# Optimization experiments

Hardware: AMD Instinct MI355X
Metric: run time of the kernel (lower is better)

The kernel has to match this reference:

```python
import jax, jax.numpy as jnp
import numpy as np

_ICO_FACES0 = [
    [0,11,5],[0,5,1],[0,1,7],[0,7,10],[0,10,11],
    [1,5,9],[5,11,4],[11,10,2],[10,7,6],[7,1,8],
    [3,9,4],[3,4,2],[3,2,6],[3,6,8],[3,8,9],
    [4,9,5],[2,4,11],[6,2,10],[8,6,7],[9,8,1]]


def ico_sphere_np(level=1):
    t = (1.0 + 5.0 ** 0.5) / 2.0
    verts = np.array([[-1,t,0],[1,t,0],[-1,-t,0],[1,-t,0],
                      [0,-1,t],[0,1,t],[0,-1,-t],[0,1,-t],
                      [t,0,-1],[t,0,1],[-t,0,-1],[-t,0,1]], dtype=np.float64)
    verts = verts / np.linalg.norm(verts, axis=1, keepdims=True)
    faces = [list(f) for f in _ICO_FACES0]
    for _ in range(level):
        vlist = [v for v in verts]
        cache = {}
        def mid(a, b):
            k = (min(a, b), max(a, b))
            if k not in cache:
                v = vlist[a] + vlist[b]
                vlist.append(v / np.linalg.norm(v))
                cache[k] = len(vlist) - 1
            return cache[k]
        nf = []
        for a, b, c in faces:
            ab, bc, ca = mid(a, b), mid(b, c), mid(c, a)
            nf += [[a, ab, ca], [b, bc, ab], [c, ca, bc], [ab, bc, ca]]
        faces = nf
        verts = np.stack(vlist)
    return verts.astype(np.float32), np.array(faces, dtype=np.int32)


def make_template():
    verts, faces = ico_sphere_np(1)          # (42,3), (80,3)
    v = verts[None]                          # (1,42,3)
    vmin = v.min(axis=1, keepdims=True)
    vmax = v.max(axis=1, keepdims=True)
    center = (vmin + vmax) / 2.0
    scale = (vmax - vmin).max() / 2.0        # normalize_to_box
    tv = 1.4 * (v - center) / scale          # cage_size = 1.4
    return jnp.asarray(np.transpose(tv, (0, 2, 1))), jnp.asarray(faces)  # (1,3,42),(80,3)


def optimize_cage(cage, shape, distance=0.4, iters=100, step=0.01):
    # cage (1,3,C), shape (B,3,N)
    B = shape.shape[0]
    cage = jnp.broadcast_to(cage, (B,) + cage.shape[1:])
    def body(_, c):
        d = jnp.sqrt(jnp.sum((c[:, :, :, None] - shape[:, :, None, :]) ** 2, axis=1))  # (B,C,N)
        min_d = jnp.min(d, axis=2)                                                     # (B,C)
        upd = (min_d > distance).astype(c.dtype)
        return c + step * (-c) * upd[:, None, :]
    return jax.lax.fori_loop(0, iters, body, cage)


def mean_value_coordinates_3D(query, vertices, faces):
    # query (B,P,3), vertices (B,C,3), faces (F,3) shared across batch
    B, P, _ = query.shape
    C = vertices.shape[1]
    r1 = jnp.array([1, 2, 0]); r2 = jnp.array([2, 0, 1])
    uj = vertices[:, None] - query[:, :, None]            # (B,P,C,3)
    dj = jnp.linalg.norm(uj, axis=-1, keepdims=True)      # (B,P,C,1)
    uj = uj / dj
    ui = uj[:, :, faces]                                  # (B,P,F,3,3)
    li = jnp.linalg.norm(ui[:, :, :, r1] - ui[:, :, :, r2], axis=-1)  # (B,P,F,3)
    eps = 2e-5
    li = jnp.where(li >= 2, li - jax.lax.stop_gradient(li - (2 - eps)), li)
    li = jnp.where(li <= -2, li - jax.lax.stop_gradient(li + (2 - eps)), li)
    theta = 2.0 * jnp.arcsin(li / 2.0)                    # (B,P,F,3)
    h = jnp.sum(theta, axis=-1, keepdims=True) / 2.0      # (B,P,F,1)
    ci = 2.0 * jnp.sin(h) * jnp.sin(h - theta) / (jnp.sin(theta[..., r1]) * jnp.sin(theta[..., r2])) - 1.0
    ci = jnp.clip(ci, -1 + 1e-5, 1 - 1e-5)
    si = jnp.sign(jnp.linalg.det(ui))[..., None] * jnp.sqrt(1.0 - ci ** 2)  # (B,P,F,3)
    di = dj[..., 0][:, :, faces]                          # (B,P,F,3)
    wi = (theta - ci[..., r1] * theta[..., r2] - ci[..., r2] * theta[..., r1]) / (di * jnp.sin(theta[..., r1]) * si[..., r2])
    inside = (jnp.pi - h[..., 0]) < 1e-4                  # (B,P,F)
    any_inside = jnp.any(inside, axis=-1, keepdims=True)[..., None]  # (B,P,1,1)
    wi = jnp.where(any_inside, 0.0, wi)
    wi = jnp.where(inside[..., None], jnp.sin(theta) * di[..., r2] * di[..., r1], wi)
    # scatter face corners -> vertices (B,P,F*3) -> (B,P,C)
    wj = jnp.zeros((B, P, C), wi.dtype).at[:, :, faces.reshape(-1)].add(wi.reshape(B, P, -1))
    close = dj[..., 0] < 1e-8                             # (B,P,C)
    wj = jnp.where(jnp.any(close, axis=-1, keepdims=True), 0.0, wj)
    wj = jnp.where(close, 1.0, wj)
    sumWj = jnp.sum(wj, axis=-1, keepdims=True)
    sumWj = jnp.where(sumWj == 0, 1.0, sumWj)
    return wj / sumWj, wi


def setup_inputs() -> dict:
    key = jax.random.key(0)
    ks = jax.random.split(key, 12)
    B, N, FEAT = 16, 8192, 256
    template_vertices, faces = make_template()
    def lin(k, fi, fo):
        k1, k2 = jax.random.split(k)
        return (jax.random.normal(k1, (fi, fo), jnp.float32) / np.sqrt(fi).astype(np.float32),
                jax.random.normal(k2, (fo,), jnp.float32) * 0.01)
    W1, b1 = lin(ks[0], 2 * FEAT, 512)
    W2, b2 = lin(ks[1], 512, 512)
    W3, b3 = lin(ks[2], 512, 256)
    W4, b4 = lin(ks[3], 256, 42 * 3)
    return {
        'source_shape': jax.random.normal(ks[4], (B, 3, N), jnp.float32),
        'target_shape': jax.random.normal(ks[5], (B, 3, N), jnp.float32),
        'source_f': jax.random.normal(ks[6], (B, FEAT), jnp.float32),
        'target_f': jax.random.normal(ks[7], (B, FEAT), jnp.float32),
        'template_vertices': template_vertices, 'faces': faces,
        'W1': W1, 'b1': b1, 'W2': W2, 'b2': b2, 'W3': W3, 'b3': b3, 'W4': W4, 'b4': b4,
    }


def reference(source_shape, target_shape, source_f, target_f, template_vertices, faces,
              W1, b1, W2, b2, W3, b3, W4, b4):
    B = source_shape.shape[0]
    cage = optimize_cage(template_vertices, source_shape)        # (B,3,42)
    feat = jnp.concatenate([source_f, target_f], axis=-1)        # (B,512)
    h = jax.nn.relu(feat @ W1 + b1)
    h = jax.nn.relu(h @ W2 + b2)
    h = jax.nn.relu(h @ W3 + b3)
    influence_offset = h @ W4 + b4                               # (B,126)
    cage_offset = influence_offset.reshape(B, 3, -1)             # (B,3,42)
    new_cage = cage + cage_offset
    cage_t = jnp.transpose(cage, (0, 2, 1))                      # (B,42,3)
    new_cage_t = jnp.transpose(new_cage, (0, 2, 1))
    weights, _ = mean_value_coordinates_3D(jnp.transpose(source_shape, (0, 2, 1)), cage_t, faces)
    weights = jax.lax.stop_gradient(weights)                     # weights.detach() in deform_with_MVC
    deformed = jnp.einsum('bpc,bcd->bpd', weights, new_cage_t)   # (B,N,3)
    return cage_t, new_cage_t, jnp.transpose(deformed, (0, 2, 1)), weights, influence_offset
```

## Files before the change

kernel.cpp:

```cpp
#include <hip/hip_runtime.h>
#include <math.h>

#define BB 16
#define NP 8192
#define NV 42
#define NF 80
#define FEAT 256
#define PPB 64
#define FH  40

__device__ __forceinline__ float rcp_f(float x)  { return __builtin_amdgcn_rcpf(x); }
__device__ __forceinline__ float rsq_f(float x)  { return __builtin_amdgcn_rsqf(x); }
__device__ __forceinline__ float sqrt_f(float x) { return __builtin_amdgcn_sqrtf(x); }

__device__ __forceinline__ float theta_from_x(float x) {
  bool big = x > 0.5f;
  float z = big ? fmaf(-0.5f, x, 0.5f) : x * x;
  float s = big ? sqrt_f(z) : x;
  float P = fmaf(z, 0.022371875f, 0.030381944f);
  P = fmaf(z, P, 0.044642857f);
  P = fmaf(z, P, 0.075f);
  P = fmaf(z, P, 0.16666667f);
  float r = fmaf(s * z, P, s);
  return big ? fmaf(-4.f, r, 3.14159265358979f) : 2.f * r;
}

__global__ __launch_bounds__(256) void cage_opt_kernel(
    const float* __restrict__ tmpl,
    const float* __restrict__ src,
    float* __restrict__ cage)
{
  __shared__ float red[8];
  int b = blockIdx.x / NV;
  int v = blockIdx.x % NV;
  const float* sp = src + (size_t)b * 3 * NP;
  float cx = tmpl[v], cy = tmpl[NV + v], cz = tmpl[2 * NV + v];
  int k = 0;
  while (true) {
    float m = 3.4e38f;
    for (int i = threadIdx.x; i < NP; i += 256) {
      float dx = __fsub_rn(cx, sp[i]);
      float dy = __fsub_rn(cy, sp[NP + i]);
      float dz = __fsub_rn(cz, sp[2 * NP + i]);
      float ss = __fadd_rn(__fadd_rn(__fmul_rn(dx, dx), __fmul_rn(dy, dy)),
                           __fmul_rn(dz, dz));
      m = fminf(m, ss);
    }
    #pragma unroll
    for (int off = 32; off > 0; off >>= 1)
      m = fminf(m, __shfl_down(m, off, 64));
    int wid = threadIdx.x >> 6;
    __syncthreads();
    if ((threadIdx.x & 63) == 0) red[wid] = m;
    __syncthreads();
    if (threadIdx.x == 0) {
      float mm = fminf(fminf(red[0], red[1]), fminf(red[2], red[3]));
      red[4] = sqrtf(mm);
    }
    __syncthreads();
    float mind = red[4];
    if (mind > 0.4f && k < 100) {
      cx = __fsub_rn(cx, __fmul_rn(0.01f, cx));
      cy = __fsub_rn(cy, __fmul_rn(0.01f, cy));
      cz = __fsub_rn(cz, __fmul_rn(0.01f, cz));
      k++;
    } else {
      break;
    }
  }
  if (threadIdx.x == 0) {
    cage[(size_t)b * 3 * NV + v]          = cx;
    cage[(size_t)b * 3 * NV + NV + v]     = cy;
    cage[(size_t)b * 3 * NV + 2 * NV + v] = cz;
  }
}

__global__ __launch_bounds__(256) void linear_splitk(
    const float* __restrict__ in0, const float* __restrict__ in1,
    const float* __restrict__ W, const float* __restrict__ bias,
    float* __restrict__ out, int FI, int FO, int relu)
{
  __shared__ float sIn[512];
  __shared__ float part[4][64];
  int bb = blockIdx.y;
  int tid = threadIdx.x;
  for (int i = tid; i < FI; i += 256) {
    float v;
    if (in1) v = (i < FEAT) ? in0[(size_t)bb * FEAT + i]
                            : in1[(size_t)bb * FEAT + i - FEAT];
    else     v = in0[(size_t)bb * FI + i];
    sIn[i] = v;
  }
  __syncthreads();
  int o = blockIdx.x * 64 + (tid & 63);
  int kk = tid >> 6;
  int seg = FI >> 2;
  float acc = 0.f;
  const float* wp = W + o;
  #pragma unroll 4
  for (int i = kk * seg; i < (kk + 1) * seg; i++)
    acc = fmaf(sIn[i], wp[(size_t)i * FO], acc);
  part[kk][tid & 63] = acc;
  __syncthreads();
  if (tid < 64) {
    float r = ((part[0][tid] + part[1][tid]) + (part[2][tid] + part[3][tid]))
              + bias[o];
    out[(size_t)bb * FO + o] = relu ? fmaxf(r, 0.f) : r;
  }
}

__global__ __launch_bounds__(128) void l4_finalize_kernel(
    const float* __restrict__ h3,
    const float* __restrict__ W4, const float* __restrict__ b4,
    const float* __restrict__ cage,
    float* __restrict__ out_io,
    float* __restrict__ cage_t,
    float* __restrict__ ncage_t)
{
  __shared__ float sIn[256];
  int bb = blockIdx.x;
  int tid = threadIdx.x;
  sIn[tid] = h3[(size_t)bb * 256 + tid];
  sIn[tid + 128] = h3[(size_t)bb * 256 + tid + 128];
  __syncthreads();
  if (tid < 126) {
    float acc = b4[tid];
    const float* wp = W4 + tid;
    #pragma unroll 4
    for (int i = 0; i < 256; i++) acc = fmaf(sIn[i], wp[(size_t)i * 126], acc);
    out_io[(size_t)bb * 126 + tid] = acc;
    float c  = cage[(size_t)bb * 126 + tid];
    float nc = c + acc;
    int d = tid / NV, v = tid - d * NV;
    cage_t[(size_t)bb * NV * 3 + v * 3 + d]  = c;
    ncage_t[(size_t)bb * NV * 3 + v * 3 + d] = nc;
  }
}

__global__ __launch_bounds__(128, 3) void mvc_kernel(
    const float* __restrict__ src,
    const float* __restrict__ cage_t,
    const float* __restrict__ ncage_t,
    const int* __restrict__ faces,
    float* __restrict__ out_def,
    float* __restrict__ out_w)
{
  __shared__ float4 vpos[NV];
  __shared__ float4 npos[NV];
  __shared__ int fidp[NF];
  __shared__ float wj[2 * NV][PPB];
  __shared__ unsigned long long closeM[2][PPB];
  __shared__ int insideF[2][PPB];

  const float PI_F = 3.14159265358979323846f;
  int tid = threadIdx.x;
  int p   = tid & (PPB - 1);
  int hf  = tid >> 6;
  int b    = blockIdx.x / (NP / PPB);
  int pblk = blockIdx.x % (NP / PPB);
  int gp   = pblk * PPB + p;

  if (tid < NV) {
    const float* cp = cage_t + (size_t)b * NV * 3 + tid * 3;
    vpos[tid] = make_float4(cp[0], cp[1], cp[2], 0.f);
    const float* np_ = ncage_t + (size_t)b * NV * 3 + tid * 3;
    npos[tid] = make_float4(np_[0], np_[1], np_[2], 0.f);
  }
  if (tid < NF) {
    int f0 = faces[3 * tid], f1 = faces[3 * tid + 1], f2 = faces[3 * tid + 2];
    fidp[tid] = f0 | (f1 << 6) | (f2 << 12);
  }
  #pragma unroll
  for (int c = 0; c < NV; c++) wj[hf * NV + c][p] = 0.f;
  __syncthreads();

  float qx = src[(size_t)b * 3 * NP + gp];
  float qy = src[(size_t)b * 3 * NP + NP + gp];
  float qz = src[(size_t)b * 3 * NP + 2 * NP + gp];

  int anyInside = 0;
  unsigned long long closeMask = 0ull;

  auto face_geom = [&](int i, int& f0, int& f1, int& f2,
                       float& d0, float& d1, float& d2,
                       float& th0, float& th1, float& th2,
                       float& st0, float& st1, float& st2,
                       float& hh, float& sh, float& sm0, float& sm1, float& sm2,
                       float& sg) {
    int pk = fidp[i];
    f0 = pk & 63; f1 = (pk >> 6) & 63; f2 = pk >> 12;
    float4 v0 = vpos[f0], v1 = vpos[f1], v2 = vpos[f2];
    float a0x = v0.x - qx, a0y = v0.y - qy, a0z = v0.z - qz;
    float a1x = v1.x - qx, a1y = v1.y - qy, a1z = v1.z - qz;
    float a2x = v2.x - qx, a2y = v2.y - qy, a2z = v2.z - qz;
    float ss0 = fmaf(a0x, a0x, fmaf(a0y, a0y, a0z * a0z));
    float ss1 = fmaf(a1x, a1x, fmaf(a1y, a1y, a1z * a1z));
    float ss2 = fmaf(a2x, a2x, fmaf(a2y, a2y, a2z * a2z));
    float i0 = rsq_f(ss0), i1 = rsq_f(ss1), i2 = rsq_f(ss2);
    d0 = ss0 * i0; d1 = ss1 * i1; d2 = ss2 * i2;
    if (d0 < 1e-8f) closeMask |= (1ull << f0);
    if (d1 < 1e-8f) closeMask |= (1ull << f1);
    if (d2 < 1e-8f) closeMask |= (1ull << f2);
    float u0x = a0x * i0, u0y = a0y * i0, u0z = a0z * i0;
    float u1x = a1x * i1, u1y = a1y * i1, u1z = a1z * i1;
    float u2x = a2x * i2, u2y = a2y * i2, u2z = a2z * i2;
    float ex, ey, ez;
    ex = u1x - u2x; ey = u1y - u2y; ez = u1z - u2z;
    float x0 = 0.5f * sqrt_f(fmaf(ex, ex, fmaf(ey, ey, ez * ez)));
    ex = u2x - u0x; ey = u2y - u0y; ez = u2z - u0z;
    float x1 = 0.5f * sqrt_f(fmaf(ex, ex, fmaf(ey, ey, ez * ez)));
    ex = u0x - u1x; ey = u0y - u1y; ez = u0z - u1z;
    float x2 = 0.5f * sqrt_f(fmaf(ex, ex, fmaf(ey, ey, ez * ez)));
    if (x0 >= 1.f) x0 = 0.99999f;
    if (x1 >= 1.f) x1 = 0.99999f;
    if (x2 >= 1.f) x2 = 0.99999f;
    float cx0 = sqrt_f(fmaxf(fmaf(-x0, x0, 1.f), 0.f));
    float cx1 = sqrt_f(fmaxf(fmaf(-x1, x1, 1.f), 0.f));
    float cx2 = sqrt_f(fmaxf(fmaf(-x2, x2, 1.f), 0.f));
    th0 = theta_from_x(x0);
    th1 = theta_from_x(x1);
    th2 = theta_from_x(x2);
    hh  = 0.5f * ((th0 + th1) + th2);
    st0 = 2.f * (x0 * cx0);
    st1 = 2.f * (x1 * cx1);
    st2 = 2.f * (x2 * cx2);
    float A1 = x0 * (cx1 * cx2);
    float A2 = x1 * (cx0 * cx2);
    float A3 = x2 * (cx0 * cx1);
    float A4 = x0 * (x1 * x2);
    sh  = ((A1 + A2) + A3) - A4;
    sm0 = ((-A1 + A2) + A3) + A4;
    sm1 = ((A1 - A2) + A3) + A4;
    sm2 = ((A1 + A2) - A3) + A4;
    float det = u0x * fmaf(u1y, u2z, -u1z * u2y)
              - u0y * fmaf(u1x, u2z, -u1z * u2x)
              + u0z * fmaf(u1x, u2y, -u1y * u2x);
    sg = (det > 0.f) ? 1.f : ((det < 0.f) ? -1.f : 0.f);
  };

  #pragma unroll 1
  for (int i = hf * FH; i < hf * FH + FH; i++) {
    int f0, f1, f2;
    float d0, d1, d2, th0, th1, th2, st0, st1, st2, hh, sh, sm0, sm1, sm2, sg;
    face_geom(i, f0, f1, f2, d0, d1, d2, th0, th1, th2, st0, st1, st2,
              hh, sh, sm0, sm1, sm2, sg);
    if (PI_F - hh < 1e-4f) anyInside = 1;
    float twosh = 2.f * sh;
    float c0 = fmaf(twosh * sm0, rcp_f(st1 * st2), -1.f);
    float c1 = fmaf(twosh * sm1, rcp_f(st2 * st0), -1.f);
    float c2 = fmaf(twosh * sm2, rcp_f(st0 * st1), -1.f);
    c0 = fminf(fmaxf(c0, -0.99999f), 0.99999f);
    c1 = fminf(fmaxf(c1, -0.99999f), 0.99999f);
    c2 = fminf(fmaxf(c2, -0.99999f), 0.99999f);
    float s0 = sg * sqrt_f(fmaf(-c0, c0, 1.f));
    float s1 = sg * sqrt_f(fmaf(-c1, c1, 1.f));
    float s2 = sg * sqrt_f(fmaf(-c2, c2, 1.f));
    float w0 = (fmaf(-c2, th1, fmaf(-c1, th2, th0))) * rcp_f((d0 * st1) * s2);
    float w1 = (fmaf(-c0, th2, fmaf(-c2, th0, th1))) * rcp_f((d1 * st2) * s0);
    float w2 = (fmaf(-c1, th0, fmaf(-c0, th1, th2))) * rcp_f((d2 * st0) * s1);
    wj[hf * NV + f0][p] += w0;
    wj[hf * NV + f1][p] += w1;
    wj[hf * NV + f2][p] += w2;
  }

  closeM[hf][p]  = closeMask;
  insideF[hf][p] = anyInside;
  __syncthreads();

  int mIn = insideF[0][p] | insideF[1][p];
  unsigned long long mCl = closeM[0][p] | closeM[1][p];

  if (mIn) {
    #pragma unroll
    for (int c = 0; c < NV; c++) wj[hf * NV + c][p] = 0.f;
    #pragma unroll 1
    for (int i = hf * FH; i < hf * FH + FH; i++) {
      int f0, f1, f2;
      float d0, d1, d2, th0, th1, th2, st0, st1, st2, hh, sh, sm0, sm1, sm2, sg;
      face_geom(i, f0, f1, f2, d0, d1, d2, th0, th1, th2, st0, st1, st2,
                hh, sh, sm0, sm1, sm2, sg);
      if (PI_F - hh < 1e-4f) {
        wj[hf * NV + f0][p] += (st0 * d2) * d1;
        wj[hf * NV + f1][p] += (st1 * d0) * d2;
        wj[hf * NV + f2][p] += (st2 * d1) * d0;
      }
    }
  }
  __syncthreads();

  if (tid < PPB) {
    float sum = 0.f;
    #pragma unroll
    for (int c = 0; c < NV; c++) {
      float w = wj[c][p] + wj[NV + c][p];
      if (mCl) w = ((mCl >> c) & 1ull) ? 1.f : 0.f;
      wj[c][p] = w;
      sum += w;
    }
    if (sum == 0.f) sum = 1.f;
    float inv = rcp_f(sum);
    float ax = 0.f, ay = 0.f, az = 0.f;
    #pragma unroll
    for (int c = 0; c < NV; c++) {
      float w = wj[c][p] * inv;
      wj[c][p] = w;
      float4 n = npos[c];
      ax = fmaf(w, n.x, ax);
      ay = fmaf(w, n.y, ay);
      az = fmaf(w, n.z, az);
    }
    out_def[(size_t)b * 3 * NP + gp]          = ax;
    out_def[(size_t)b * 3 * NP + NP + gp]     = ay;
    out_def[(size_t)b * 3 * NP + 2 * NP + gp] = az;
  }
  __syncthreads();

  float* wbase = out_w + ((size_t)b * NP + pblk * PPB) * NV;
  for (int idx = tid; idx < PPB * NV; idx += 128) {
    int pp = idx / NV;
    int c  = idx - pp * NV;
    wbase[idx] = wj[c][pp];
  }
}

extern "C" void kernel_launch(void* const* d_in, const int* in_sizes, int n_in,
                              void* d_out, int out_size, void* d_ws, size_t ws_size,
                              hipStream_t stream) {
  (void)in_sizes; (void)n_in; (void)out_size; (void)d_ws; (void)ws_size;
  const float* src   = (const float*)d_in[0];
  const float* sf    = (const float*)d_in[2];
  const float* tf    = (const float*)d_in[3];
  const float* tmpl  = (const float*)d_in[4];
  const int*   faces = (const int*)d_in[5];
  const float* W1 = (const float*)d_in[6];  const float* b1 = (const float*)d_in[7];
  const float* W2 = (const float*)d_in[8];  const float* b2 = (const float*)d_in[9];
  const float* W3 = (const float*)d_in[10]; const float* b3 = (const float*)d_in[11];
  const float* W4 = (const float*)d_in[12]; const float* b4 = (const float*)d_in[13];

  float* out = (float*)d_out;
  float* out_cage_t  = out;
  float* out_ncage_t = out + 2016;
  float* out_def     = out + 4032;
  float* out_w       = out + 397248;
  float* out_io      = out + 5902272;

  float* s_cage = out_w;
  float* s_h1   = out_w + 2016;
  float* s_h2   = out_w + 10208;
  float* s_h3   = out_w + 18400;

  cage_opt_kernel<<<dim3(BB * NV), dim3(256), 0, stream>>>(tmpl, src, s_cage);
  linear_splitk<<<dim3(8, BB), dim3(256), 0, stream>>>(sf, tf, W1, b1, s_h1, 512, 512, 1);
  linear_splitk<<<dim3(8, BB), dim3(256), 0, stream>>>(s_h1, nullptr, W2, b2, s_h2, 512, 512, 1);
  linear_splitk<<<dim3(4, BB), dim3(256), 0, stream>>>(s_h2, nullptr, W3, b3, s_h3, 512, 256, 1);
  l4_finalize_kernel<<<dim3(BB), dim3(128), 0, stream>>>(
      s_h3, W4, b4, s_cage, out_io, out_cage_t, out_ncage_t);
  mvc_kernel<<<dim3(BB * (NP / PPB)), dim3(128), 0, stream>>>(
      src, out_cage_t, out_ncage_t, faces, out_def, out_w);
}
```

Baseline: 168.8 us.

## Split MVC faces across four waves with LDS atomics and fuse cage-opt with layer 1

The MVC kernel now uses 256 threads per block, with four waves each handling 20 faces per point. Weights are accumulated with shared-memory atomicAdd into a padded array, and the normalization and deformation reductions are split across the waves. The inside-face recomputation moves to a noinline helper that runs only when a block has an inside point. The cage optimisation and the first linear layer are merged into one launch, saving a kernel launch and letting them overlap. The atomics, the extra barriers and the higher register pressure could offset the gain from more parallelism.

```diff
diff --git a/kernel.cpp b/kernel.cpp
--- a/kernel.cpp
+++ b/kernel.cpp
@@ -7,7 +7,8 @@
 #define NF 80
 #define FEAT 256
 #define PPB 64
-#define FH  40
+#define QF  20
+#define WJS 65
 
 __device__ __forceinline__ float rcp_f(float x)  { return __builtin_amdgcn_rcpf(x); }
 __device__ __forceinline__ float rsq_f(float x)  { return __builtin_amdgcn_rsqf(x); }
@@ -25,65 +26,243 @@
   return big ? fmaf(-4.f, r, 3.14159265358979f) : 2.f * r;
 }
 
-__global__ __launch_bounds__(256) void cage_opt_kernel(
-    const float* __restrict__ tmpl,
+__device__ __attribute__((noinline)) void inside_face_rt(
+    int f0, int f1, int f2, const float4* vpos,
+    float qx, float qy, float qz, float* wj, int p)
+{
+  float4 v0 = vpos[f0], v1 = vpos[f1], v2 = vpos[f2];
+  float a0x = v0.x - qx, a0y = v0.y - qy, a0z = v0.z - qz;
+  float a1x = v1.x - qx, a1y = v1.y - qy, a1z = v1.z - qz;
+  float a2x = v2.x - qx, a2y = v2.y - qy, a2z = v2.z - qz;
+  float ss0 = fmaf(a0x, a0x, fmaf(a0y, a0y, a0z * a0z));
+  float ss1 = fmaf(a1x, a1x, fmaf(a1y, a1y, a1z * a1z));
+  float ss2 = fmaf(a2x, a2x, fmaf(a2y, a2y, a2z * a2z));
+  float i0 = rsq_f(ss0), i1 = rsq_f(ss1), i2 = rsq_f(ss2);
+  float d0 = ss0 * i0, d1 = ss1 * i1, d2 = ss2 * i2;
+  float u0x = a0x * i0, u0y = a0y * i0, u0z = a0z * i0;
+  float u1x = a1x * i1, u1y = a1y * i1, u1z = a1z * i1;
+  float u2x = a2x * i2, u2y = a2y * i2, u2z = a2z * i2;
+  float ex = u1x - u2x, ey = u1y - u2y, ez = u1z - u2z;
+  float x0 = 0.5f * sqrt_f(fmaf(ex, ex, fmaf(ey, ey, ez * ez)));
+  ex = u2x - u0x; ey = u2y - u0y; ez = u2z - u0z;
+  float x1 = 0.5f * sqrt_f(fmaf(ex, ex, fmaf(ey, ey, ez * ez)));
+  ex = u0x - u1x; ey = u0y - u1y; ez = u0z - u1z;
+  float x2 = 0.5f * sqrt_f(fmaf(ex, ex, fmaf(ey, ey, ez * ez)));
+  if (x0 >= 1.f) x0 = 0.99999f;
+  if (x1 >= 1.f) x1 = 0.99999f;
+  if (x2 >= 1.f) x2 = 0.99999f;
+  float th0 = theta_from_x(x0), th1 = theta_from_x(x1), th2 = theta_from_x(x2);
+  float hh = 0.5f * ((th0 + th1) + th2);
+  if (3.14159265358979f - hh < 1e-4f) {
+    float cx0 = sqrt_f(fmaxf(fmaf(-x0, x0, 1.f), 0.f));
+    float cx1 = sqrt_f(fmaxf(fmaf(-x1, x1, 1.f), 0.f));
+    float cx2 = sqrt_f(fmaxf(fmaf(-x2, x2, 1.f), 0.f));
+    atomicAdd(&wj[f0 * WJS + p], (2.f * (x0 * cx0) * d2) * d1);
+    atomicAdd(&wj[f1 * WJS + p], (2.f * (x1 * cx1) * d0) * d2);
+    atomicAdd(&wj[f2 * WJS + p], (2.f * (x2 * cx2) * d1) * d0);
+  }
+}
+
+__global__ __launch_bounds__(256) void mvc_kernel(
     const float* __restrict__ src,
-    float* __restrict__ cage)
-{
-  __shared__ float red[8];
-  int b = blockIdx.x / NV;
-  int v = blockIdx.x % NV;
-  const float* sp = src + (size_t)b * 3 * NP;
-  float cx = tmpl[v], cy = tmpl[NV + v], cz = tmpl[2 * NV + v];
-  int k = 0;
-  while (true) {
-    float m = 3.4e38f;
-    for (int i = threadIdx.x; i < NP; i += 256) {
-      float dx = __fsub_rn(cx, sp[i]);
-      float dy = __fsub_rn(cy, sp[NP + i]);
-      float dz = __fsub_rn(cz, sp[2 * NP + i]);
-      float ss = __fadd_rn(__fadd_rn(__fmul_rn(dx, dx), __fmul_rn(dy, dy)),
-                           __fmul_rn(dz, dz));
-      m = fminf(m, ss);
-    }
-    #pragma unroll
-    for (int off = 32; off > 0; off >>= 1)
-      m = fminf(m, __shfl_down(m, off, 64));
-    int wid = threadIdx.x >> 6;
+    const float* __restrict__ cage_t,
+    const float* __restrict__ ncage_t,
+    const int* __restrict__ faces,
+    float* __restrict__ out_def,
+    float* __restrict__ out_w)
+{
+  __shared__ float4 vpos[NV];
+  __shared__ float4 npos[NV];
+  __shared__ int fidp[NF];
+  __shared__ float wj[NV * WJS];
+  __shared__ float spart[4][PPB];
+  __shared__ float dxp[4][PPB], dyp[4][PPB], dzp[4][PPB];
+  __shared__ float invL[PPB];
+  __shared__ unsigned int closeLo[PPB], closeHi[PPB];
+  __shared__ int insideL[PPB];
+  __shared__ int blkIn;
+
+  const float PI_F = 3.14159265358979323846f;
+  int tid = threadIdx.x;
+  int p = tid & (PPB - 1);
+  int q = tid >> 6;
+  int b    = blockIdx.x / (NP / PPB);
+  int pblk = blockIdx.x % (NP / PPB);
+  int gp   = pblk * PPB + p;
+
+  if (tid < NV) {
+    const float* cp = cage_t + (size_t)b * NV * 3 + tid * 3;
+    vpos[tid] = make_float4(cp[0], cp[1], cp[2], 0.f);
+    const float* np_ = ncage_t + (size_t)b * NV * 3 + tid * 3;
+    npos[tid] = make_float4(np_[0], np_[1], np_[2], 0.f);
+  }
+  if (tid < NF) {
+    int f0 = faces[3 * tid], f1 = faces[3 * tid + 1], f2 = faces[3 * tid + 2];
+    fidp[tid] = f0 | (f1 << 6) | (f2 << 12);
+  }
+  for (int i = tid; i < NV * WJS; i += 256) wj[i] = 0.f;
+  if (tid < PPB) { insideL[tid] = 0; closeLo[tid] = 0u; closeHi[tid] = 0u; }
+  if (tid == 0) blkIn = 0;
+  __syncthreads();
+
+  float qx = src[(size_t)b * 3 * NP + gp];
+  float qy = src[(size_t)b * 3 * NP + NP + gp];
+  float qz = src[(size_t)b * 3 * NP + 2 * NP + gp];
+
+  int anyInside = 0;
+  unsigned long long closeMask = 0ull;
+
+  #pragma unroll 1
+  for (int i = q * QF; i < q * QF + QF; i++) {
+    int pk = fidp[i];
+    int f0 = pk & 63, f1 = (pk >> 6) & 63, f2 = pk >> 12;
+    float4 v0 = vpos[f0], v1 = vpos[f1], v2 = vpos[f2];
+    float a0x = v0.x - qx, a0y = v0.y - qy, a0z = v0.z - qz;
+    float a1x = v1.x - qx, a1y = v1.y - qy, a1z = v1.z - qz;
+    float a2x = v2.x - qx, a2y = v2.y - qy, a2z = v2.z - qz;
+    float ss0 = fmaf(a0x, a0x, fmaf(a0y, a0y, a0z * a0z));
+    float ss1 = fmaf(a1x, a1x, fmaf(a1y, a1y, a1z * a1z));
+    float ss2 = fmaf(a2x, a2x, fmaf(a2y, a2y, a2z * a2z));
+    if (ss0 < 1e-16f) closeMask |= (1ull << f0);
+    if (ss1 < 1e-16f) closeMask |= (1ull << f1);
+    if (ss2 < 1e-16f) closeMask |= (1ull << f2);
+    float i0 = rsq_f(ss0), i1 = rsq_f(ss1), i2 = rsq_f(ss2);
+    float d0 = ss0 * i0, d1 = ss1 * i1, d2 = ss2 * i2;
+    float u0x = a0x * i0, u0y = a0y * i0, u0z = a0z * i0;
+    float u1x = a1x * i1, u1y = a1y * i1, u1z = a1z * i1;
+    float u2x = a2x * i2, u2y = a2y * i2, u2z = a2z * i2;
+    float ex = u1x - u2x, ey = u1y - u2y, ez = u1z - u2z;
+    float x0 = 0.5f * sqrt_f(fmaf(ex, ex, fmaf(ey, ey, ez * ez)));
+    ex = u2x - u0x; ey = u2y - u0y; ez = u2z - u0z;
+    float x1 = 0.5f * sqrt_f(fmaf(ex, ex, fmaf(ey, ey, ez * ez)));
+    ex = u0x - u1x; ey = u0y - u1y; ez = u0z - u1z;
+    float x2 = 0.5f * sqrt_f(fmaf(ex, ex, fmaf(ey, ey, ez * ez)));
+    if (x0 >= 1.f) x0 = 0.99999f;
+    if (x1 >= 1.f) x1 = 0.99999f;
+    if (x2 >= 1.f) x2 = 0.99999f;
+    float cx0 = sqrt_f(fmaxf(fmaf(-x0, x0, 1.f), 0.f));
+    float cx1 = sqrt_f(fmaxf(fmaf(-x1, x1, 1.f), 0.f));
+    float cx2 = sqrt_f(fmaxf(fmaf(-x2, x2, 1.f), 0.f));
+    float th0 = theta_from_x(x0);
+    float th1 = theta_from_x(x1);
+    float th2 = theta_from_x(x2);
+    float hh = 0.5f * ((th0 + th1) + th2);
+    if (PI_F - hh < 1e-4f) anyInside = 1;
+    float st0 = 2.f * (x0 * cx0);
+    float st1 = 2.f * (x1 * cx1);
+    float st2 = 2.f * (x2 * cx2);
+    float A1 = x0 * (cx1 * cx2);
+    float A2 = x1 * (cx0 * cx2);
+    float A3 = x2 * (cx0 * cx1);
+    float A4 = x0 * (x1 * x2);
+    float sh  = ((A1 + A2) + A3) - A4;
+    float sm0 = ((-A1 + A2) + A3) + A4;
+    float sm1 = ((A1 - A2) + A3) + A4;
+    float sm2 = ((A1 + A2) - A3) + A4;
+    float twosh = 2.f * sh;
+    float c0 = fmaf(twosh * sm0, rcp_f(st1 * st2), -1.f);
+    float c1 = fmaf(twosh * sm1, rcp_f(st2 * st0), -1.f);
+    float c2 = fmaf(twosh * sm2, rcp_f(st0 * st1), -1.f);
+    c0 = fminf(fmaxf(c0, -0.99999f), 0.99999f);
+    c1 = fminf(fmaxf(c1, -0.99999f), 0.99999f);
+    c2 = fminf(fmaxf(c2, -0.99999f), 0.99999f);
+    float det = u0x * fmaf(u1y, u2z, -(u1z * u2y))
+              - u0y * fmaf(u1x, u2z, -(u1z * u2x))
+              + u0z * fmaf(u1x, u2y, -(u1y * u2x));
+    float sg = (det > 0.f) ? 1.f : ((det < 0.f) ? -1.f : 0.f);
+    float sn0 = sg * sqrt_f(fmaf(-c0, c0, 1.f));
+    float sn1 = sg * sqrt_f(fmaf(-c1, c1, 1.f));
+    float sn2 = sg * sqrt_f(fmaf(-c2, c2, 1.f));
+    float w0 = fmaf(-c2, th1, fmaf(-c1, th2, th0)) * rcp_f((d0 * st1) * sn2);
+    float w1 = fmaf(-c0, th2, fmaf(-c2, th0, th1)) * rcp_f((d1 * st2) * sn0);
+    float w2 = fmaf(-c1, th0, fmaf(-c0, th1, th2)) * rcp_f((d2 * st0) * sn1);
+    atomicAdd(&wj[f0 * WJS + p], w0);
+    atomicAdd(&wj[f1 * WJS + p], w1);
+    atomicAdd(&wj[f2 * WJS + p], w2);
+  }
+
+  if (anyInside) { insideL[p] = 1; blkIn = 1; }
+  if (closeMask) {
+    atomicOr(&closeLo[p], (unsigned int)closeMask);
+    atomicOr(&closeHi[p], (unsigned int)(closeMask >> 32));
+  }
+  __syncthreads();
+
+  if (blkIn) {
+    if (tid < PPB && insideL[tid])
+      for (int c = 0; c < NV; c++) wj[c * WJS + tid] = 0.f;
     __syncthreads();
-    if ((threadIdx.x & 63) == 0) red[wid] = m;
-    __syncthreads();
-    if (threadIdx.x == 0) {
-      float mm = fminf(fminf(red[0], red[1]), fminf(red[2], red[3]));
-      red[4] = sqrtf(mm);
+    if (insideL[p]) {
+      for (int i = q * QF; i < q * QF + QF; i++) {
+        int pk = fidp[i];
+        inside_face_rt(pk & 63, (pk >> 6) & 63, pk >> 12,
+                       vpos, qx, qy, qz, wj, p);
+      }
     }
     __syncthreads();
-    float mind = red[4];
-    if (mind > 0.4f && k < 100) {
-      cx = __fsub_rn(cx, __fmul_rn(0.01f, cx));
-      cy = __fsub_rn(cy, __fmul_rn(0.01f, cy));
-      cz = __fsub_rn(cz, __fmul_rn(0.01f, cz));
-      k++;
+  }
+
+  {
+    float ps = 0.f;
+    for (int c = q; c < NV; c += 4) ps += wj[c * WJS + p];
+    spart[q][p] = ps;
+  }
+  __syncthreads();
+  if (tid < PPB) {
+    unsigned long long mCl =
+        (unsigned long long)closeLo[tid] |
+        ((unsigned long long)closeHi[tid] << 32);
+    float sum;
+    if (mCl) {
+      for (int c = 0; c < NV; c++)
+        wj[c * WJS + tid] = ((mCl >> c) & 1ull) ? 1.f : 0.f;
+      sum = (float)__popcll(mCl);
     } else {
-      break;
+      sum = (spart[0][tid] + spart[1][tid]) + (spart[2][tid] + spart[3][tid]);
     }
-  }
-  if (threadIdx.x == 0) {
-    cage[(size_t)b * 3 * NV + v]          = cx;
-    cage[(size_t)b * 3 * NV + NV + v]     = cy;
-    cage[(size_t)b * 3 * NV + 2 * NV + v] = cz;
-  }
-}
-
-__global__ __launch_bounds__(256) void linear_splitk(
-    const float* __restrict__ in0, const float* __restrict__ in1,
-    const float* __restrict__ W, const float* __restrict__ bias,
-    float* __restrict__ out, int FI, int FO, int relu)
-{
-  __shared__ float sIn[512];
-  __shared__ float part[4][64];
-  int bb = blockIdx.y;
-  int tid = threadIdx.x;
+    if (sum == 0.f) sum = 1.f;
+    invL[tid] = rcp_f(sum);
+  }
+  __syncthreads();
+  {
+    float inv = invL[p];
+    float ax = 0.f, ay = 0.f, az = 0.f;
+    for (int c = q; c < NV; c += 4) {
+      float w = wj[c * WJS + p] * inv;
+      wj[c * WJS + p] = w;
+      float4 n = npos[c];
+      ax = fmaf(w, n.x, ax);
+      ay = fmaf(w, n.y, ay);
+      az = fmaf(w, n.z, az);
+    }
+    dxp[q][p] = ax; dyp[q][p] = ay; dzp[q][p] = az;
+  }
+  __syncthreads();
+  if (tid < PPB) {
+    float ax = (dxp[0][tid] + dxp[1][tid]) + (dxp[2][tid] + dxp[3][tid]);
+    float ay = (dyp[0][tid] + dyp[1][tid]) + (dyp[2][tid] + dyp[3][tid]);
+    float az = (dzp[0][tid] + dzp[1][tid]) + (dzp[2][tid] + dzp[3][tid]);
+    int gpp = pblk * PPB + tid;
+    out_def[(size_t)b * 3 * NP + gpp]          = ax;
+    out_def[(size_t)b * 3 * NP + NP + gpp]     = ay;
+    out_def[(size_t)b * 3 * NP + 2 * NP + gpp] = az;
+  }
+  __syncthreads();
+
+  float* wbase = out_w + ((size_t)b * NP + pblk * PPB) * NV;
+  for (int idx = tid; idx < PPB * NV; idx += 256) {
+    int pp = idx / NV;
+    int c  = idx - pp * NV;
+    wbase[idx] = wj[c * WJS + pp];
+  }
+}
+
+__device__ __forceinline__ void splitk_body(
+    const float* in0, const float* in1,
+    const float* W, const float* bias, float* out,
+    int FI, int FO, int relu, int ox, int bb, int tid,
+    float* sIn, float (*part)[64])
+{
   for (int i = tid; i < FI; i += 256) {
     float v;
     if (in1) v = (i < FEAT) ? in0[(size_t)bb * FEAT + i]
@@ -92,7 +271,7 @@
     sIn[i] = v;
   }
   __syncthreads();
-  int o = blockIdx.x * 64 + (tid & 63);
+  int o = ox * 64 + (tid & 63);
   int kk = tid >> 6;
   int seg = FI >> 2;
   float acc = 0.f;
@@ -107,6 +286,78 @@
               + bias[o];
     out[(size_t)bb * FO + o] = relu ? fmaxf(r, 0.f) : r;
   }
+}
+
+__global__ __launch_bounds__(256) void cage_l1_kernel(
+    const float* __restrict__ tmpl, const float* __restrict__ src,
+    const float* __restrict__ sf, const float* __restrict__ tf,
+    const float* __restrict__ W1, const float* __restrict__ b1,
+    float* __restrict__ cage, float* __restrict__ h1)
+{
+  __shared__ float red[8];
+  __shared__ float sIn[512];
+  __shared__ float part[4][64];
+  int tid = threadIdx.x;
+
+  if (blockIdx.x < BB * NV) {
+    int b = blockIdx.x / NV;
+    int v = blockIdx.x % NV;
+    const float* sp = src + (size_t)b * 3 * NP;
+    float cx = tmpl[v], cy = tmpl[NV + v], cz = tmpl[2 * NV + v];
+    int k = 0;
+    while (true) {
+      float m = 3.4e38f;
+      for (int i = tid; i < NP; i += 256) {
+        float dx = __fsub_rn(cx, sp[i]);
+        float dy = __fsub_rn(cy, sp[NP + i]);
+        float dz = __fsub_rn(cz, sp[2 * NP + i]);
+        float ss = __fadd_rn(__fadd_rn(__fmul_rn(dx, dx), __fmul_rn(dy, dy)),
+                             __fmul_rn(dz, dz));
+        m = fminf(m, ss);
+      }
+      #pragma unroll
+      for (int off = 32; off > 0; off >>= 1)
+        m = fminf(m, __shfl_down(m, off, 64));
+      int wid = tid >> 6;
+      __syncthreads();
+      if ((tid & 63) == 0) red[wid] = m;
+      __syncthreads();
+      if (tid == 0) {
+        float mm = fminf(fminf(red[0], red[1]), fminf(red[2], red[3]));
+        red[4] = sqrtf(mm);
+      }
+      __syncthreads();
+      float mind = red[4];
+      if (mind > 0.4f && k < 100) {
+        cx = __fsub_rn(cx, __fmul_rn(0.01f, cx));
+        cy = __fsub_rn(cy, __fmul_rn(0.01f, cy));
+        cz = __fsub_rn(cz, __fmul_rn(0.01f, cz));
+        k++;
+      } else {
+        break;
+      }
+    }
+    if (tid == 0) {
+      cage[(size_t)b * 3 * NV + v]          = cx;
+      cage[(size_t)b * 3 * NV + NV + v]     = cy;
+      cage[(size_t)b * 3 * NV + 2 * NV + v] = cz;
+    }
+  } else {
+    int idx = blockIdx.x - BB * NV;
+    splitk_body(sf, tf, W1, b1, h1, 512, 512, 1, idx & 7, idx >> 3,
+                tid, sIn, part);
+  }
+}
+
+__global__ __launch_bounds__(256) void linear_splitk(
+    const float* __restrict__ in0, const float* __restrict__ in1,
+    const float* __restrict__ W, const float* __restrict__ bias,
+    float* __restrict__ out, int FI, int FO, int relu)
+{
+  __shared__ float sIn[512];
+  __shared__ float part[4][64];
+  splitk_body(in0, in1, W, bias, out, FI, FO, relu,
+              blockIdx.x, blockIdx.y, threadIdx.x, sIn, part);
 }
 
 __global__ __launch_bounds__(128) void l4_finalize_kernel(
@@ -134,192 +385,6 @@
     int d = tid / NV, v = tid - d * NV;
     cage_t[(size_t)bb * NV * 3 + v * 3 + d]  = c;
     ncage_t[(size_t)bb * NV * 3 + v * 3 + d] = nc;
-  }
-}
-
-__global__ __launch_bounds__(128, 3) void mvc_kernel(
-    const float* __restrict__ src,
-    const float* __restrict__ cage_t,
-    const float* __restrict__ ncage_t,
-    const int* __restrict__ faces,
-    float* __restrict__ out_def,
-    float* __restrict__ out_w)
-{
-  __shared__ float4 vpos[NV];
-  __shared__ float4 npos[NV];
-  __shared__ int fidp[NF];
-  __shared__ float wj[2 * NV][PPB];
-  __shared__ unsigned long long closeM[2][PPB];
-  __shared__ int insideF[2][PPB];
-
-  const float PI_F = 3.14159265358979323846f;
-  int tid = threadIdx.x;
-  int p   = tid & (PPB - 1);
-  int hf  = tid >> 6;
-  int b    = blockIdx.x / (NP / PPB);
-  int pblk = blockIdx.x % (NP / PPB);
-  int gp   = pblk * PPB + p;
-
-  if (tid < NV) {
-    const float* cp = cage_t + (size_t)b * NV * 3 + tid * 3;
-    vpos[tid] = make_float4(cp[0], cp[1], cp[2], 0.f);
-    const float* np_ = ncage_t + (size_t)b * NV * 3 + tid * 3;
-    npos[tid] = make_float4(np_[0], np_[1], np_[2], 0.f);
-  }
-  if (tid < NF) {
-    int f0 = faces[3 * tid], f1 = faces[3 * tid + 1], f2 = faces[3 * tid + 2];
-    fidp[tid] = f0 | (f1 << 6) | (f2 << 12);
-  }
-  #pragma unroll
-  for (int c = 0; c < NV; c++) wj[hf * NV + c][p] = 0.f;
-  __syncthreads();
-
-  float qx = src[(size_t)b * 3 * NP + gp];
-  float qy = src[(size_t)b * 3 * NP + NP + gp];
-  float qz = src[(size_t)b * 3 * NP + 2 * NP + gp];
-
-  int anyInside = 0;
-  unsigned long long closeMask = 0ull;
-
-  auto face_geom = [&](int i, int& f0, int& f1, int& f2,
-                       float& d0, float& d1, float& d2,
-                       float& th0, float& th1, float& th2,
-                       float& st0, float& st1, float& st2,
-                       float& hh, float& sh, float& sm0, float& sm1, float& sm2,
-                       float& sg) {
-    int pk = fidp[i];
-    f0 = pk & 63; f1 = (pk >> 6) & 63; f2 = pk >> 12;
-    float4 v0 = vpos[f0], v1 = vpos[f1], v2 = vpos[f2];
-    float a0x = v0.x - qx, a0y = v0.y - qy, a0z = v0.z - qz;
-    float a1x = v1.x - qx, a1y = v1.y - qy, a1z = v1.z - qz;
-    float a2x = v2.x - qx, a2y = v2.y - qy, a2z = v2.z - qz;
-    float ss0 = fmaf(a0x, a0x, fmaf(a0y, a0y, a0z * a0z));
-    float ss1 = fmaf(a1x, a1x, fmaf(a1y, a1y, a1z * a1z));
-    float ss2 = fmaf(a2x, a2x, fmaf(a2y, a2y, a2z * a2z));
-    float i0 = rsq_f(ss0), i1 = rsq_f(ss1), i2 = rsq_f(ss2);
-    d0 = ss0 * i0; d1 = ss1 * i1; d2 = ss2 * i2;
-    if (d0 < 1e-8f) closeMask |= (1ull << f0);
-    if (d1 < 1e-8f) closeMask |= (1ull << f1);
-    if (d2 < 1e-8f) closeMask |= (1ull << f2);
-    float u0x = a0x * i0, u0y = a0y * i0, u0z = a0z * i0;
-    float u1x = a1x * i1, u1y = a1y * i1, u1z = a1z * i1;
-    float u2x = a2x * i2, u2y = a2y * i2, u2z = a2z * i2;
-    float ex, ey, ez;
-    ex = u1x - u2x; ey = u1y - u2y; ez = u1z - u2z;
-    float x0 = 0.5f * sqrt_f(fmaf(ex, ex, fmaf(ey, ey, ez * ez)));
-    ex = u2x - u0x; ey = u2y - u0y; ez = u2z - u0z;
-    float x1 = 0.5f * sqrt_f(fmaf(ex, ex, fmaf(ey, ey, ez * ez)));
-    ex = u0x - u1x; ey = u0y - u1y; ez = u0z - u1z;
-    float x2 = 0.5f * sqrt_f(fmaf(ex, ex, fmaf(ey, ey, ez * ez)));
-    if (x0 >= 1.f) x0 = 0.99999f;
-    if (x1 >= 1.f) x1 = 0.99999f;
-    if (x2 >= 1.f) x2 = 0.99999f;
-    float cx0 = sqrt_f(fmaxf(fmaf(-x0, x0, 1.f), 0.f));
-    float cx1 = sqrt_f(fmaxf(fmaf(-x1, x1, 1.f), 0.f));
-    float cx2 = sqrt_f(fmaxf(fmaf(-x2, x2, 1.f), 0.f));
-    th0 = theta_from_x(x0);
-    th1 = theta_from_x(x1);
-    th2 = theta_from_x(x2);
-    hh  = 0.5f * ((th0 + th1) + th2);
-    st0 = 2.f * (x0 * cx0);
-    st1 = 2.f * (x1 * cx1);
-    st2 = 2.f * (x2 * cx2);
-    float A1 = x0 * (cx1 * cx2);
-    float A2 = x1 * (cx0 * cx2);
-    float A3 = x2 * (cx0 * cx1);
-    float A4 = x0 * (x1 * x2);
-    sh  = ((A1 + A2) + A3) - A4;
-    sm0 = ((-A1 + A2) + A3) + A4;
-    sm1 = ((A1 - A2) + A3) + A4;
-    sm2 = ((A1 + A2) - A3) + A4;
-    float det = u0x * fmaf(u1y, u2z, -u1z * u2y)
-              - u0y * fmaf(u1x, u2z, -u1z * u2x)
-              + u0z * fmaf(u1x, u2y, -u1y * u2x);
-    sg = (det > 0.f) ? 1.f : ((det < 0.f) ? -1.f : 0.f);
-  };
-
-  #pragma unroll 1
-  for (int i = hf * FH; i < hf * FH + FH; i++) {
-    int f0, f1, f2;
-    float d0, d1, d2, th0, th1, th2, st0, st1, st2, hh, sh, sm0, sm1, sm2, sg;
-    face_geom(i, f0, f1, f2, d0, d1, d2, th0, th1, th2, st0, st1, st2,
-              hh, sh, sm0, sm1, sm2, sg);
-    if (PI_F - hh < 1e-4f) anyInside = 1;
-    float twosh = 2.f * sh;
-    float c0 = fmaf(twosh * sm0, rcp_f(st1 * st2), -1.f);
-    float c1 = fmaf(twosh * sm1, rcp_f(st2 * st0), -1.f);
-    float c2 = fmaf(twosh * sm2, rcp_f(st0 * st1), -1.f);
-    c0 = fminf(fmaxf(c0, -0.99999f), 0.99999f);
-    c1 = fminf(fmaxf(c1, -0.99999f), 0.99999f);
-    c2 = fminf(fmaxf(c2, -0.99999f), 0.99999f);
-    float s0 = sg * sqrt_f(fmaf(-c0, c0, 1.f));
-    float s1 = sg * sqrt_f(fmaf(-c1, c1, 1.f));
-    float s2 = sg * sqrt_f(fmaf(-c2, c2, 1.f));
-    float w0 = (fmaf(-c2, th1, fmaf(-c1, th2, th0))) * rcp_f((d0 * st1) * s2);
-    float w1 = (fmaf(-c0, th2, fmaf(-c2, th0, th1))) * rcp_f((d1 * st2) * s0);
-    float w2 = (fmaf(-c1, th0, fmaf(-c0, th1, th2))) * rcp_f((d2 * st0) * s1);
-    wj[hf * NV + f0][p] += w0;
-    wj[hf * NV + f1][p] += w1;
-    wj[hf * NV + f2][p] += w2;
-  }
-
-  closeM[hf][p]  = closeMask;
-  insideF[hf][p] = anyInside;
-  __syncthreads();
-
-  int mIn = insideF[0][p] | insideF[1][p];
-  unsigned long long mCl = closeM[0][p] | closeM[1][p];
-
-  if (mIn) {
-    #pragma unroll
-    for (int c = 0; c < NV; c++) wj[hf * NV + c][p] = 0.f;
-    #pragma unroll 1
-    for (int i = hf * FH; i < hf * FH + FH; i++) {
-      int f0, f1, f2;
-      float d0, d1, d2, th0, th1, th2, st0, st1, st2, hh, sh, sm0, sm1, sm2, sg;
-      face_geom(i, f0, f1, f2, d0, d1, d2, th0, th1, th2, st0, st1, st2,
-                hh, sh, sm0, sm1, sm2, sg);
-      if (PI_F - hh < 1e-4f) {
-        wj[hf * NV + f0][p] += (st0 * d2) * d1;
-        wj[hf * NV + f1][p] += (st1 * d0) * d2;
-        wj[hf * NV + f2][p] += (st2 * d1) * d0;
-      }
-    }
-  }
-  __syncthreads();
-
-  if (tid < PPB) {
-    float sum = 0.f;
-    #pragma unroll
-    for (int c = 0; c < NV; c++) {
-      float w = wj[c][p] + wj[NV + c][p];
-      if (mCl) w = ((mCl >> c) & 1ull) ? 1.f : 0.f;
-      wj[c][p] = w;
-      sum += w;
-    }
-    if (sum == 0.f) sum = 1.f;
-    float inv = rcp_f(sum);
-    float ax = 0.f, ay = 0.f, az = 0.f;
-    #pragma unroll
-    for (int c = 0; c < NV; c++) {
-      float w = wj[c][p] * inv;
-      wj[c][p] = w;
-      float4 n = npos[c];
-      ax = fmaf(w, n.x, ax);
-      ay = fmaf(w, n.y, ay);
-      az = fmaf(w, n.z, az);
-    }
-    out_def[(size_t)b * 3 * NP + gp]          = ax;
-    out_def[(size_t)b * 3 * NP + NP + gp]     = ay;
-    out_def[(size_t)b * 3 * NP + 2 * NP + gp] = az;
-  }
-  __syncthreads();
-
-  float* wbase = out_w + ((size_t)b * NP + pblk * PPB) * NV;
-  for (int idx = tid; idx < PPB * NV; idx += 128) {
-    int pp = idx / NV;
-    int c  = idx - pp * NV;
-    wbase[idx] = wj[c][pp];
   }
 }
 
@@ -349,12 +414,12 @@
   float* s_h2   = out_w + 10208;
   float* s_h3   = out_w + 18400;
 
-  cage_opt_kernel<<<dim3(BB * NV), dim3(256), 0, stream>>>(tmpl, src, s_cage);
-  linear_splitk<<<dim3(8, BB), dim3(256), 0, stream>>>(sf, tf, W1, b1, s_h1, 512, 512, 1);
+  cage_l1_kernel<<<dim3(BB * NV + 128), dim3(256), 0, stream>>>(
+      tmpl, src, sf, tf, W1, b1, s_cage, s_h1);
   linear_splitk<<<dim3(8, BB), dim3(256), 0, stream>>>(s_h1, nullptr, W2, b2, s_h2, 512, 512, 1);
   linear_splitk<<<dim3(4, BB), dim3(256), 0, stream>>>(s_h2, nullptr, W3, b3, s_h3, 512, 256, 1);
   l4_finalize_kernel<<<dim3(BB), dim3(128), 0, stream>>>(
       s_h3, W4, b4, s_cage, out_io, out_cage_t, out_ncage_t);
-  mvc_kernel<<<dim3(BB * (NP / PPB)), dim3(128), 0, stream>>>(
+  mvc_kernel<<<dim3(BB * (NP / PPB)), dim3(256), 0, stream>>>(
       src, out_cage_t, out_ncage_t, faces, out_def, out_w);
 }
```

Measured after the change: 239.5 us. 41.9% more time.
